# Kernel tuning notes

Measured on AMD Instinct MI355X. Metric: run time of the kernel, lower is better.

## Reference

```python
import jax, jax.numpy as jnp
import numpy as np

B, S, D, H = 2, 4096, 512, 8
DH = D // H  # head dim = 64

def setup_inputs() -> dict:
    key = jax.random.key(0)
    ks = jax.random.split(key, 9)
    s = 0.02
    return {
        "Q": jax.random.normal(ks[0], (B, S, D), jnp.float32),
        "Wq": jax.random.normal(ks[1], (D, D), jnp.float32) * s,
        "bq": jnp.zeros((D,), jnp.float32),
        "Wk": jax.random.normal(ks[2], (D, D), jnp.float32) * s,
        "bk": jnp.zeros((D,), jnp.float32),
        "Wv": jax.random.normal(ks[3], (D, D), jnp.float32) * s,
        "bv": jnp.zeros((D,), jnp.float32),
        "Wo": jax.random.normal(ks[4], (D, D), jnp.float32) * s,
        "bo": jnp.zeros((D,), jnp.float32),
    }

def reference(Q, Wq, bq, Wk, bk, Wv, bv, Wo, bo):
    bs, s, d = Q.shape
    scale = DH ** -0.5
    # torch Linear: x @ W.T + b, W is [out, in]
    q = (Q @ Wq.T + bq).reshape(bs, s, H, DH).transpose(0, 2, 1, 3)  # [b,h,s,dh]
    k = (Q @ Wk.T + bk).reshape(bs, s, H, DH).transpose(0, 2, 1, 3)
    v = (Q @ Wv.T + bv).reshape(bs, s, H, DH).transpose(0, 2, 1, 3)
    scores = jnp.einsum('bhqd,bhkd->bhqk', q, k) * scale  # [b,h,s,s]
    attn = jax.nn.softmax(scores, axis=-1)
    out = jnp.einsum('bhqk,bhkd->bhqd', attn, v)  # [b,h,s,dh]
    out = out.transpose(0, 2, 1, 3).reshape(bs, s, H * DH)
    out = out @ Wo.T + bo
    return (out, attn)
```

## Files before the change

kernel.cpp:

```cpp
#include <hip/hip_runtime.h>
#include <hip/hip_bf16.h>

#define B_  2
#define S_  4096
#define D_  512
#define H_  8
#define DH_ 64
#define BH_ 16
#define M_  (B_*S_)

typedef __attribute__((ext_vector_type(4))) float f32x4;
typedef __attribute__((ext_vector_type(8))) short s16x8;
typedef __attribute__((ext_vector_type(4))) short s16x4;

#define MFMA(A,Bv,C) __builtin_amdgcn_mfma_f32_16x16x32_bf16(A,Bv,C,0,0,0)

typedef const void __attribute__((address_space(1)))* gas_t;
typedef void __attribute__((address_space(3)))* las_t;
#define GLDS(gp, lp) __builtin_amdgcn_global_load_lds((gas_t)(gp), (las_t)(lp), 16, 0, 0)

#define EXP_C 0.18033688011112042f

static __device__ __forceinline__ unsigned short f2bf(float f){
    union { __hip_bfloat16 h; unsigned short u; } v;
    v.h = __float2bfloat16(f);
    return v.u;
}
static __device__ __forceinline__ float bf2f(unsigned short b){
    union { unsigned int u; float f; } v; v.u = ((unsigned int)b) << 16;
    return v.f;
}

__global__ __launch_bounds__(256) void cvt_w4(const float* __restrict__ s0, const float* __restrict__ s1,
                                              const float* __restrict__ s2, const float* __restrict__ s3,
                                              unsigned short* __restrict__ d0, unsigned short* __restrict__ d1,
                                              unsigned short* __restrict__ d2, unsigned short* __restrict__ d3){
    const float* s; unsigned short* d;
    switch (blockIdx.y){
        case 0: s = s0; d = d0; break;
        case 1: s = s1; d = d1; break;
        case 2: s = s2; d = d2; break;
        default: s = s3; d = d3; break;
    }
    int i = blockIdx.x * 256 + threadIdx.x;
    float4 v = reinterpret_cast<const float4*>(s)[i];
    ushort4 o;
    o.x = f2bf(v.x); o.y = f2bf(v.y); o.z = f2bf(v.z); o.w = f2bf(v.w);
    reinterpret_cast<ushort4*>(d)[i] = o;
}

__global__ __launch_bounds__(512, 4) void gemm_qkv(const float* __restrict__ Q,
                                                   const unsigned short* __restrict__ Wq, const float* __restrict__ bq,
                                                   const unsigned short* __restrict__ Wk, const float* __restrict__ bk,
                                                   const unsigned short* __restrict__ Wv, const float* __restrict__ bv,
                                                   unsigned short* __restrict__ qh, unsigned short* __restrict__ kh,
                                                   unsigned short* __restrict__ vT){
    __shared__ unsigned short tile[128][65];
    const int mt = blockIdx.x, h = blockIdx.y;
    const int wave = threadIdx.x >> 6, lane = threadIdx.x & 63;
    const int g = lane >> 4, r16 = lane & 15;
    const int b  = mt >> 5;
    const int s0 = (mt & 31) * 128;

    s16x8 areg[16];
    {
        const float* Arow = Q + (size_t)(mt*128 + wave*16 + r16) * 512;
        #pragma unroll
        for (int j = 0; j < 8; ++j){
            float4 l0 = *(const float4*)(Arow + j*64 + g*8);
            float4 l1 = *(const float4*)(Arow + j*64 + g*8 + 4);
            float4 h0 = *(const float4*)(Arow + j*64 + 32 + g*8);
            float4 h1 = *(const float4*)(Arow + j*64 + 32 + g*8 + 4);
            union { s16x8 v; unsigned short u[8]; } t0, t1;
            t0.u[0]=f2bf(l0.x); t0.u[1]=f2bf(l0.y); t0.u[2]=f2bf(l0.z); t0.u[3]=f2bf(l0.w);
            t0.u[4]=f2bf(l1.x); t0.u[5]=f2bf(l1.y); t0.u[6]=f2bf(l1.z); t0.u[7]=f2bf(l1.w);
            t1.u[0]=f2bf(h0.x); t1.u[1]=f2bf(h0.y); t1.u[2]=f2bf(h0.z); t1.u[3]=f2bf(h0.w);
            t1.u[4]=f2bf(h1.x); t1.u[5]=f2bf(h1.y); t1.u[6]=f2bf(h1.z); t1.u[7]=f2bf(h1.w);
            areg[2*j]   = t0.v;
            areg[2*j+1] = t1.v;
        }
    }

    #pragma unroll 1
    for (int w = 0; w < 3; ++w){
        const unsigned short* W = (w==0)?Wq:(w==1)?Wk:Wv;
        const float* bias       = (w==0)?bq:(w==1)?bk:bv;

        f32x4 acc[4];
        #pragma unroll
        for (int i = 0; i < 4; ++i) acc[i] = (f32x4){0.f,0.f,0.f,0.f};

        #pragma unroll
        for (int j = 0; j < 8; ++j){
            #pragma unroll
            for (int nt = 0; nt < 4; ++nt){
                const unsigned short* Wp = W + (size_t)(h*64 + nt*16 + r16)*512 + j*64 + g*8;
                s16x8 b0 = *(const s16x8*)(Wp);
                s16x8 b1 = *(const s16x8*)(Wp + 32);
                acc[nt] = MFMA(areg[2*j],   b0, acc[nt]);
                acc[nt] = MFMA(areg[2*j+1], b1, acc[nt]);
            }
        }

        if (w < 2){
            unsigned short* dst = (w==0) ? qh : kh;
            #pragma unroll
            for (int nt = 0; nt < 4; ++nt){
                const float bv_ = bias[h*64 + nt*16 + r16];
                #pragma unroll
                for (int r = 0; r < 4; ++r){
                    const int s = s0 + wave*16 + g*4 + r;
                    dst[((size_t)(b*H_ + h)*S_ + s)*DH_ + nt*16 + r16] = f2bf(acc[nt][r] + bv_);
                }
            }
        } else {
            #pragma unroll
            for (int nt = 0; nt < 4; ++nt){
                const float bv_ = bias[h*64 + nt*16 + r16];
                #pragma unroll
                for (int r = 0; r < 4; ++r)
                    tile[wave*16 + g*4 + r][nt*16 + r16] = f2bf(acc[nt][r] + bv_);
            }
            __syncthreads();
            const int c = threadIdx.x & 127, r4 = threadIdx.x >> 7;
            unsigned short* dst = vT + (size_t)(b*H_ + h)*DH_*S_;
            #pragma unroll
            for (int i = 0; i < 16; ++i){
                const int dh = i*4 + r4;
                dst[(size_t)dh*S_ + s0 + c] = tile[c][dh];
            }
        }
    }
}

__global__ __launch_bounds__(512, 4) void gemm_o(const unsigned short* __restrict__ A,
                                                 const unsigned short* __restrict__ W,
                                                 const float* __restrict__ bias,
                                                 float* __restrict__ dst){
    const int mt = blockIdx.x, nt0 = blockIdx.y;
    const int wave = threadIdx.x >> 6, lane = threadIdx.x & 63;
    const int g = lane >> 4, r16 = lane & 15;

    s16x8 areg[16];
    {
        const unsigned short* Arow = A + (size_t)(mt*128 + wave*16 + r16) * 512;
        #pragma unroll
        for (int j = 0; j < 8; ++j){
            areg[2*j]   = *(const s16x8*)(Arow + j*64 + g*8);
            areg[2*j+1] = *(const s16x8*)(Arow + j*64 + 32 + g*8);
        }
    }

    f32x4 acc[4];
    #pragma unroll
    for (int i = 0; i < 4; ++i) acc[i] = (f32x4){0.f,0.f,0.f,0.f};

    #pragma unroll
    for (int j = 0; j < 8; ++j){
        #pragma unroll
        for (int nt = 0; nt < 4; ++nt){
            const unsigned short* Wp = W + (size_t)(nt0*64 + nt*16 + r16)*512 + j*64 + g*8;
            s16x8 b0 = *(const s16x8*)(Wp);
            s16x8 b1 = *(const s16x8*)(Wp + 32);
            acc[nt] = MFMA(areg[2*j],   b0, acc[nt]);
            acc[nt] = MFMA(areg[2*j+1], b1, acc[nt]);
        }
    }

    #pragma unroll
    for (int nt = 0; nt < 4; ++nt){
        const float bv = bias[nt0*64 + nt*16 + r16];
        #pragma unroll
        for (int r = 0; r < 4; ++r){
            const int orow = mt*128 + wave*16 + g*4 + r;
            dst[(size_t)orow*512 + nt0*64 + nt*16 + r16] = acc[nt][r] + bv;
        }
    }
}

__global__ __launch_bounds__(512, 4) void attn_fused(const unsigned short* __restrict__ qh,
                                                     const unsigned short* __restrict__ kh,
                                                     const unsigned short* __restrict__ vT,
                                                     float* __restrict__ attn,
                                                     unsigned short* __restrict__ ctx){
    __shared__ unsigned short Kb[3][64][64];
    __shared__ unsigned short Vb[2][64][64];
    __shared__ __align__(16) unsigned short Pbf[8][16][136];

    const int lin = blockIdx.y * 32 + blockIdx.x;
    const int nl  = (lin & 7) * 64 + (lin >> 3);
    const int qt  = nl & 31;
    const int bh  = nl >> 5;

    const int wave = threadIdx.x >> 6, lane = threadIdx.x & 63;
    const int g = lane >> 4, r16 = lane & 15;

    const unsigned short* qbase = qh + (size_t)bh*S_*DH_;
    const unsigned short* kbase = kh + (size_t)bh*S_*DH_;
    const unsigned short* vbase = vT + (size_t)bh*DH_*S_;

    const int tr = wave*8 + (lane >> 3);
    const int cc = (lane & 7) ^ (tr & 7);
    const int stg = tr*64 + (lane & 7)*8;

    const int sw = r16 & 7;
    const int c0 = (g ^ sw) * 8;
    const int c1 = ((4 + g) ^ sw) * 8;

    const int qrow = qt*128 + wave*16 + r16;
    s16x8 qa0 = *(const s16x8*)(qbase + (size_t)qrow*DH_ + g*8);
    s16x8 qa1 = *(const s16x8*)(qbase + (size_t)qrow*DH_ + 32 + g*8);

    GLDS(kbase + (size_t)tr*DH_ + cc*8,          &Kb[0][0][0] + stg);
    GLDS(kbase + (size_t)(64 + tr)*DH_ + cc*8,   &Kb[1][0][0] + stg);

    float lsum[4] = {0.f,0.f,0.f,0.f};
    for (int t = 0; t < 64; ++t){
        if (t == 63) asm volatile("s_waitcnt vmcnt(0)" ::: "memory");
        else         asm volatile("s_waitcnt vmcnt(1)" ::: "memory");
        __builtin_amdgcn_s_barrier();
        __builtin_amdgcn_sched_barrier(0);
        if (t < 62){
            GLDS(kbase + (size_t)((t+2)*64 + tr)*DH_ + cc*8, &Kb[(t+2)%3][0][0] + stg);
        }
        __builtin_amdgcn_sched_barrier(0);
        const unsigned short (*Kt)[64] = Kb[t % 3];
        #pragma unroll
        for (int nt = 0; nt < 4; ++nt){
            const int row = nt*16 + r16;
            s16x8 b0 = *(const s16x8*)(&Kt[row][c0]);
            s16x8 b1 = *(const s16x8*)(&Kt[row][c1]);
            f32x4 acc = (f32x4){0.f,0.f,0.f,0.f};
            acc = MFMA(qa0, b0, acc);
            acc = MFMA(qa1, b1, acc);
            #pragma unroll
            for (int r = 0; r < 4; ++r)
                lsum[r] += __builtin_amdgcn_exp2f(acc[r]*EXP_C);
        }
    }

    #pragma unroll
    for (int m = 1; m < 16; m <<= 1){
        #pragma unroll
        for (int r = 0; r < 4; ++r) lsum[r] += __shfl_xor(lsum[r], m, 64);
    }
    float inv[4];
    #pragma unroll
    for (int r = 0; r < 4; ++r) inv[r] = 1.0f / lsum[r];

    __builtin_amdgcn_s_barrier();
    __builtin_amdgcn_sched_barrier(0);
    GLDS(kbase + (size_t)tr*DH_ + cc*8,        &Kb[0][0][0] + stg);
    GLDS(vbase + (size_t)tr*S_  + cc*8,        &Vb[0][0][0] + stg);
    GLDS(kbase + (size_t)(64 + tr)*DH_ + cc*8, &Kb[1][0][0] + stg);
    asm volatile("s_waitcnt vmcnt(1)" ::: "memory");
    __builtin_amdgcn_s_barrier();
    __builtin_amdgcn_sched_barrier(0);

    f32x4 oacc[4];
    #pragma unroll
    for (int i = 0; i < 4; ++i) oacc[i] = (f32x4){0.f,0.f,0.f,0.f};

    float* attnW = attn + ((size_t)bh*S_ + qt*128 + wave*16)*S_;
    unsigned short (*Pw)[136] = Pbf[wave];
    const int sl = lane & 31, sh = lane >> 5;

    auto compute_tile = [&](int t, int ks, int vs){
        const unsigned short (*Kt)[64] = Kb[ks];
        const unsigned short (*Vt)[64] = Vb[vs];
        const int cb = (t&1)*64;
        f32x4 pacc[4];
        #pragma unroll
        for (int nt = 0; nt < 4; ++nt){
            const int row = nt*16 + r16;
            s16x8 b0 = *(const s16x8*)(&Kt[row][c0]);
            s16x8 b1 = *(const s16x8*)(&Kt[row][c1]);
            f32x4 acc = (f32x4){0.f,0.f,0.f,0.f};
            acc = MFMA(qa0, b0, acc);
            acc = MFMA(qa1, b1, acc);
            pacc[nt] = acc;
        }
        #pragma unroll
        for (int nt = 0; nt < 4; ++nt){
            #pragma unroll
            for (int r = 0; r < 4; ++r){
                float p = __builtin_amdgcn_exp2f(pacc[nt][r]*EXP_C) * inv[r];
                Pw[g*4 + r][cb + nt*16 + r16] = f2bf(p);
            }
        }
        s16x8 pa0 = *(const s16x8*)(&Pw[r16][cb + g*8]);
        s16x8 pa1 = *(const s16x8*)(&Pw[r16][cb + 32 + g*8]);
        #pragma unroll
        for (int nt = 0; nt < 4; ++nt){
            const int row = nt*16 + r16;
            s16x8 v0 = *(const s16x8*)(&Vt[row][c0]);
            s16x8 v1 = *(const s16x8*)(&Vt[row][c1]);
            oacc[nt] = MFMA(pa0, v0, oacc[nt]);
            oacc[nt] = MFMA(pa1, v1, oacc[nt]);
        }
    };

    auto store_pair = [&](int tfirst){
        #pragma unroll
        for (int i = 0; i < 8; ++i){
            const int row = i*2 + sh;
            s16x4 pb = *(const s16x4*)(&Pw[row][sl*4]);
            f32x4 o;
            #pragma unroll
            for (int j = 0; j < 4; ++j) o[j] = bf2f((unsigned short)pb[j]);
            __builtin_nontemporal_store(o,
                (f32x4*)(attnW + (size_t)row*S_ + tfirst*64 + sl*4));
        }
    };

    for (int t = 0; t < 64; ++t){
        if (t + 1 <= 63)
            GLDS(vbase + (size_t)tr*S_ + (t+1)*64 + cc*8, &Vb[(t+1)&1][0][0] + stg);
        if (t + 2 <= 63)
            GLDS(kbase + (size_t)((t+2)*64 + tr)*DH_ + cc*8, &Kb[(t+2)%3][0][0] + stg);
        __builtin_amdgcn_sched_barrier(0);
        if (t >= 2 && (t & 1) == 0){
            store_pair(t - 2);
            __builtin_amdgcn_sched_barrier(0);
        }
        compute_tile(t, t % 3, t & 1);
        if (t < 63){
            if (t == 62)            asm volatile("s_waitcnt vmcnt(8)" ::: "memory");
            else if ((t & 1) == 0 && t >= 2)
                                    asm volatile("s_waitcnt vmcnt(9)" ::: "memory");
            else                    asm volatile("s_waitcnt vmcnt(1)" ::: "memory");
            __builtin_amdgcn_s_barrier();
            __builtin_amdgcn_sched_barrier(0);
        }
    }
    store_pair(62);

    const int b = bh >> 3, h = bh & 7;
    #pragma unroll
    for (int nt = 0; nt < 4; ++nt){
        #pragma unroll
        for (int r = 0; r < 4; ++r){
            const int qr = qt*128 + wave*16 + g*4 + r;
            ctx[(size_t)(b*S_ + qr)*D_ + h*64 + nt*16 + r16] = f2bf(oacc[nt][r]);
        }
    }
}

extern "C" void kernel_launch(void* const* d_in, const int* in_sizes, int n_in,
                              void* d_out, int out_size, void* d_ws, size_t ws_size,
                              hipStream_t stream){
    const float* Q  = (const float*)d_in[0];
    const float* Wq = (const float*)d_in[1];
    const float* bq = (const float*)d_in[2];
    const float* Wk = (const float*)d_in[3];
    const float* bk = (const float*)d_in[4];
    const float* Wv = (const float*)d_in[5];
    const float* bv = (const float*)d_in[6];
    const float* Wo = (const float*)d_in[7];
    const float* bo = (const float*)d_in[8];

    float* out  = (float*)d_out;
    float* attn = out + (size_t)M_*D_;

    unsigned short* Wqb = (unsigned short*)attn;
    unsigned short* Wkb = Wqb + 512*512;
    unsigned short* Wvb = Wkb + 512*512;

    unsigned short* qhb = (unsigned short*)d_ws;
    unsigned short* khb = qhb + (size_t)BH_*S_*DH_;
    unsigned short* vTb = khb + (size_t)BH_*S_*DH_;
    unsigned short* ctx = vTb + (size_t)BH_*S_*DH_;
    unsigned short* Wob = ctx + (size_t)M_*D_;

    cvt_w4<<<dim3(256, 4), 256, 0, stream>>>(Wq, Wk, Wv, Wo, Wqb, Wkb, Wvb, Wob);

    gemm_qkv<<<dim3(M_/128, 8), 512, 0, stream>>>(Q, Wqb, bq, Wkb, bk, Wvb, bv,
                                                  qhb, khb, vTb);

    attn_fused<<<dim3(32, BH_), 512, 0, stream>>>(qhb, khb, vTb, attn, ctx);

    gemm_o<<<dim3(M_/128, D_/64), 512, 0, stream>>>(ctx, Wob, bo, out);
}
```

Baseline: 391.4 us.

## Double per-wave query rows in attention to reuse K/V tiles across two MFMA strips

Each wave now handles 32 query rows (two 16-row strips) instead of 16, so a block covers 256 queries and the grid is halved to 256 blocks. Each K and V tile loaded into LDS is reused by twice as many MFMAs, which cuts K/V traffic and barrier count per unit of work. The cost is more registers, a larger P buffer in LDS and lower occupancy (launch bounds drop to 2), leaving half as many blocks to fill the GPU. The attention-probability stores also change from nontemporal to regular stores, and the wait counts are adjusted for the doubled store volume.

```diff
diff --git a/kernel.cpp b/kernel.cpp
--- a/kernel.cpp
+++ b/kernel.cpp
@@ -178,19 +178,19 @@
     }
 }
 
-__global__ __launch_bounds__(512, 4) void attn_fused(const unsigned short* __restrict__ qh,
+__global__ __launch_bounds__(512, 2) void attn_fused(const unsigned short* __restrict__ qh,
                                                      const unsigned short* __restrict__ kh,
                                                      const unsigned short* __restrict__ vT,
                                                      float* __restrict__ attn,
                                                      unsigned short* __restrict__ ctx){
     __shared__ unsigned short Kb[3][64][64];
     __shared__ unsigned short Vb[2][64][64];
-    __shared__ __align__(16) unsigned short Pbf[8][16][136];
-
-    const int lin = blockIdx.y * 32 + blockIdx.x;
-    const int nl  = (lin & 7) * 64 + (lin >> 3);
-    const int qt  = nl & 31;
-    const int bh  = nl >> 5;
+    __shared__ __align__(16) unsigned short Pbf[8][32][136];
+
+    const int lin = blockIdx.y * 16 + blockIdx.x;
+    const int nl  = (lin & 7) * 32 + (lin >> 3);
+    const int qt  = nl & 15;
+    const int bh  = nl >> 4;
 
     const int wave = threadIdx.x >> 6, lane = threadIdx.x & 63;
     const int g = lane >> 4, r16 = lane & 15;
@@ -207,14 +207,17 @@
     const int c0 = (g ^ sw) * 8;
     const int c1 = ((4 + g) ^ sw) * 8;
 
-    const int qrow = qt*128 + wave*16 + r16;
-    s16x8 qa0 = *(const s16x8*)(qbase + (size_t)qrow*DH_ + g*8);
-    s16x8 qa1 = *(const s16x8*)(qbase + (size_t)qrow*DH_ + 32 + g*8);
+    const int qb = qt*256 + wave*32;
+    s16x8 qaA0 = *(const s16x8*)(qbase + (size_t)(qb + r16)*DH_ + g*8);
+    s16x8 qaA1 = *(const s16x8*)(qbase + (size_t)(qb + r16)*DH_ + 32 + g*8);
+    s16x8 qaB0 = *(const s16x8*)(qbase + (size_t)(qb + 16 + r16)*DH_ + g*8);
+    s16x8 qaB1 = *(const s16x8*)(qbase + (size_t)(qb + 16 + r16)*DH_ + 32 + g*8);
 
     GLDS(kbase + (size_t)tr*DH_ + cc*8,          &Kb[0][0][0] + stg);
     GLDS(kbase + (size_t)(64 + tr)*DH_ + cc*8,   &Kb[1][0][0] + stg);
 
-    float lsum[4] = {0.f,0.f,0.f,0.f};
+    float lsumA[4] = {0.f,0.f,0.f,0.f};
+    float lsumB[4] = {0.f,0.f,0.f,0.f};
     for (int t = 0; t < 64; ++t){
         if (t == 63) asm volatile("s_waitcnt vmcnt(0)" ::: "memory");
         else         asm volatile("s_waitcnt vmcnt(1)" ::: "memory");
@@ -230,23 +233,34 @@
             const int row = nt*16 + r16;
             s16x8 b0 = *(const s16x8*)(&Kt[row][c0]);
             s16x8 b1 = *(const s16x8*)(&Kt[row][c1]);
-            f32x4 acc = (f32x4){0.f,0.f,0.f,0.f};
-            acc = MFMA(qa0, b0, acc);
-            acc = MFMA(qa1, b1, acc);
-            #pragma unroll
-            for (int r = 0; r < 4; ++r)
-                lsum[r] += __builtin_amdgcn_exp2f(acc[r]*EXP_C);
+            f32x4 aA = (f32x4){0.f,0.f,0.f,0.f};
+            aA = MFMA(qaA0, b0, aA);
+            aA = MFMA(qaA1, b1, aA);
+            f32x4 aB = (f32x4){0.f,0.f,0.f,0.f};
+            aB = MFMA(qaB0, b0, aB);
+            aB = MFMA(qaB1, b1, aB);
+            #pragma unroll
+            for (int r = 0; r < 4; ++r){
+                lsumA[r] += __builtin_amdgcn_exp2f(aA[r]*EXP_C);
+                lsumB[r] += __builtin_amdgcn_exp2f(aB[r]*EXP_C);
+            }
         }
     }
 
     #pragma unroll
     for (int m = 1; m < 16; m <<= 1){
         #pragma unroll
-        for (int r = 0; r < 4; ++r) lsum[r] += __shfl_xor(lsum[r], m, 64);
-    }
-    float inv[4];
-    #pragma unroll
-    for (int r = 0; r < 4; ++r) inv[r] = 1.0f / lsum[r];
+        for (int r = 0; r < 4; ++r){
+            lsumA[r] += __shfl_xor(lsumA[r], m, 64);
+            lsumB[r] += __shfl_xor(lsumB[r], m, 64);
+        }
+    }
+    float invA[4], invB[4];
+    #pragma unroll
+    for (int r = 0; r < 4; ++r){
+        invA[r] = 1.0f / lsumA[r];
+        invB[r] = 1.0f / lsumB[r];
+    }
 
     __builtin_amdgcn_s_barrier();
     __builtin_amdgcn_sched_barrier(0);
@@ -257,11 +271,14 @@
     __builtin_amdgcn_s_barrier();
     __builtin_amdgcn_sched_barrier(0);
 
-    f32x4 oacc[4];
-    #pragma unroll
-    for (int i = 0; i < 4; ++i) oacc[i] = (f32x4){0.f,0.f,0.f,0.f};
-
-    float* attnW = attn + ((size_t)bh*S_ + qt*128 + wave*16)*S_;
+    f32x4 oaccA[4], oaccB[4];
+    #pragma unroll
+    for (int i = 0; i < 4; ++i){
+        oaccA[i] = (f32x4){0.f,0.f,0.f,0.f};
+        oaccB[i] = (f32x4){0.f,0.f,0.f,0.f};
+    }
+
+    float* attnW = attn + ((size_t)bh*S_ + qb)*S_;
     unsigned short (*Pw)[136] = Pbf[wave];
     const int sl = lane & 31, sh = lane >> 5;
 
@@ -269,47 +286,56 @@
         const unsigned short (*Kt)[64] = Kb[ks];
         const unsigned short (*Vt)[64] = Vb[vs];
         const int cb = (t&1)*64;
-        f32x4 pacc[4];
+        f32x4 paccA[4], paccB[4];
         #pragma unroll
         for (int nt = 0; nt < 4; ++nt){
             const int row = nt*16 + r16;
             s16x8 b0 = *(const s16x8*)(&Kt[row][c0]);
             s16x8 b1 = *(const s16x8*)(&Kt[row][c1]);
-            f32x4 acc = (f32x4){0.f,0.f,0.f,0.f};
-            acc = MFMA(qa0, b0, acc);
-            acc = MFMA(qa1, b1, acc);
-            pacc[nt] = acc;
+            f32x4 aA = (f32x4){0.f,0.f,0.f,0.f};
+            aA = MFMA(qaA0, b0, aA);
+            aA = MFMA(qaA1, b1, aA);
+            paccA[nt] = aA;
+            f32x4 aB = (f32x4){0.f,0.f,0.f,0.f};
+            aB = MFMA(qaB0, b0, aB);
+            aB = MFMA(qaB1, b1, aB);
+            paccB[nt] = aB;
         }
         #pragma unroll
         for (int nt = 0; nt < 4; ++nt){
             #pragma unroll
             for (int r = 0; r < 4; ++r){
-                float p = __builtin_amdgcn_exp2f(pacc[nt][r]*EXP_C) * inv[r];
-                Pw[g*4 + r][cb + nt*16 + r16] = f2bf(p);
-            }
-        }
-        s16x8 pa0 = *(const s16x8*)(&Pw[r16][cb + g*8]);
-        s16x8 pa1 = *(const s16x8*)(&Pw[r16][cb + 32 + g*8]);
+                float pA = __builtin_amdgcn_exp2f(paccA[nt][r]*EXP_C) * invA[r];
+                Pw[g*4 + r][cb + nt*16 + r16] = f2bf(pA);
+                float pB = __builtin_amdgcn_exp2f(paccB[nt][r]*EXP_C) * invB[r];
+                Pw[16 + g*4 + r][cb + nt*16 + r16] = f2bf(pB);
+            }
+        }
+        s16x8 paA0 = *(const s16x8*)(&Pw[r16][cb + g*8]);
+        s16x8 paA1 = *(const s16x8*)(&Pw[r16][cb + 32 + g*8]);
+        s16x8 paB0 = *(const s16x8*)(&Pw[16 + r16][cb + g*8]);
+        s16x8 paB1 = *(const s16x8*)(&Pw[16 + r16][cb + 32 + g*8]);
         #pragma unroll
         for (int nt = 0; nt < 4; ++nt){
             const int row = nt*16 + r16;
             s16x8 v0 = *(const s16x8*)(&Vt[row][c0]);
             s16x8 v1 = *(const s16x8*)(&Vt[row][c1]);
-            oacc[nt] = MFMA(pa0, v0, oacc[nt]);
-            oacc[nt] = MFMA(pa1, v1, oacc[nt]);
+            oaccA[nt] = MFMA(paA0, v0, oaccA[nt]);
+            oaccA[nt] = MFMA(paA1, v1, oaccA[nt]);
+            oaccB[nt] = MFMA(paB0, v0, oaccB[nt]);
+            oaccB[nt] = MFMA(paB1, v1, oaccB[nt]);
         }
     };
 
     auto store_pair = [&](int tfirst){
         #pragma unroll
-        for (int i = 0; i < 8; ++i){
+        for (int i = 0; i < 16; ++i){
             const int row = i*2 + sh;
             s16x4 pb = *(const s16x4*)(&Pw[row][sl*4]);
             f32x4 o;
             #pragma unroll
             for (int j = 0; j < 4; ++j) o[j] = bf2f((unsigned short)pb[j]);
-            __builtin_nontemporal_store(o,
-                (f32x4*)(attnW + (size_t)row*S_ + tfirst*64 + sl*4));
+            *(f32x4*)(attnW + (size_t)row*S_ + tfirst*64 + sl*4) = o;
         }
     };
 
@@ -325,9 +351,9 @@
         }
         compute_tile(t, t % 3, t & 1);
         if (t < 63){
-            if (t == 62)            asm volatile("s_waitcnt vmcnt(8)" ::: "memory");
+            if (t == 62)            asm volatile("s_waitcnt vmcnt(16)" ::: "memory");
             else if ((t & 1) == 0 && t >= 2)
-                                    asm volatile("s_waitcnt vmcnt(9)" ::: "memory");
+                                    asm volatile("s_waitcnt vmcnt(17)" ::: "memory");
             else                    asm volatile("s_waitcnt vmcnt(1)" ::: "memory");
             __builtin_amdgcn_s_barrier();
             __builtin_amdgcn_sched_barrier(0);
@@ -340,8 +366,10 @@
     for (int nt = 0; nt < 4; ++nt){
         #pragma unroll
         for (int r = 0; r < 4; ++r){
-            const int qr = qt*128 + wave*16 + g*4 + r;
-            ctx[(size_t)(b*S_ + qr)*D_ + h*64 + nt*16 + r16] = f2bf(oacc[nt][r]);
+            const int qrA = qb + g*4 + r;
+            ctx[(size_t)(b*S_ + qrA)*D_ + h*64 + nt*16 + r16] = f2bf(oaccA[nt][r]);
+            const int qrB = qb + 16 + g*4 + r;
+            ctx[(size_t)(b*S_ + qrB)*D_ + h*64 + nt*16 + r16] = f2bf(oaccB[nt][r]);
         }
     }
 }
@@ -377,7 +405,7 @@
     gemm_qkv<<<dim3(M_/128, 8), 512, 0, stream>>>(Q, Wqb, bq, Wkb, bk, Wvb, bv,
                                                   qhb, khb, vTb);
 
-    attn_fused<<<dim3(32, BH_), 512, 0, stream>>>(qhb, khb, vTb, attn, ctx);
+    attn_fused<<<dim3(16, 16), 512, 0, stream>>>(qhb, khb, vTb, attn, ctx);
 
     gemm_o<<<dim3(M_/128, D_/64), 512, 0, stream>>>(ctx, Wob, bo, out);
 }
```

Measured after the change: 464.8 us. 18.7% more time.
